# Optimization experiments

Measured on AMD Instinct MI355X. Metric: run time of the kernel, lower is better.

The kernel has to match this reference:

```python
import jax, jax.numpy as jnp
import numpy as np
from jax import lax

P = 16        # patch spatial size (C = 3 * P * P = 768)
CH = 3        # channels per patch
H = 8         # num attention heads
EPS_BN = 1e-3 # keras BatchNormalization default epsilon
EPS_LN = 1e-3 # keras LayerNormalization default epsilon


def _layernorm(x, g, b):
    mu = jnp.mean(x, axis=-1, keepdims=True)
    var = jnp.mean(jnp.square(x - mu), axis=-1, keepdims=True)
    return (x - mu) * lax.rsqrt(var + EPS_LN) * g + b


def setup_inputs() -> dict:
    key = jax.random.key(0)
    ks = jax.random.split(key, 8)
    B, N, C, DFF = 8, 1024, 768, 3072
    s = 0.02
    return {
        "encoded_patches": jax.random.normal(ks[0], (B, N, C), jnp.float32),
        "qconv_w": jax.random.normal(ks[1], (3, 3, CH, CH), jnp.float32) * 0.2,
        "reatten_w": jax.random.normal(ks[2], (H, H), jnp.float32) * 0.3,
        "reatten_b": jnp.zeros((H,), jnp.float32),
        "bn_gamma": jnp.ones((H,), jnp.float32),
        "bn_beta": jnp.zeros((H,), jnp.float32),
        "proj_w": jax.random.normal(ks[3], (C, C), jnp.float32) * s,
        "proj_b": jnp.zeros((C,), jnp.float32),
        "ffn_w1": jax.random.normal(ks[4], (C, DFF), jnp.float32) * s,
        "ffn_b1": jnp.zeros((DFF,), jnp.float32),
        "ffn_w2": jax.random.normal(ks[5], (DFF, C), jnp.float32) * s,
        "ffn_b2": jnp.zeros((C,), jnp.float32),
        "ln1_g": jnp.ones((C,), jnp.float32),
        "ln1_b": jnp.zeros((C,), jnp.float32),
        "ln2_g": jnp.ones((C,), jnp.float32),
        "ln2_b": jnp.zeros((C,), jnp.float32),
    }


def reference(encoded_patches, qconv_w, reatten_w, reatten_b, bn_gamma, bn_beta,
              proj_w, proj_b, ffn_w1, ffn_b1, ffn_w2, ffn_b2,
              ln1_g, ln1_b, ln2_g, ln2_b):
    B, N, C = encoded_patches.shape
    hd = C // H
    scale = jnp.float32(hd) ** -0.5

    # create_queries: unflatten [B,N,C] -> [B*N,P,P,CH], 3x3 'same' conv,
    # flatten back and split heads -> [B,H,N,hd]. Source uses qconv2d for
    # q, k AND v, so q == k == v; compute once.
    y = encoded_patches.reshape(B * N, P, P, CH)
    y = lax.conv_general_dilated(y, qconv_w, (1, 1), 'SAME',
                                 dimension_numbers=('NHWC', 'HWIO', 'NHWC'))
    q = y.reshape(B, N, H, hd).transpose(0, 2, 1, 3)  # [B,H,N,hd]
    k = q
    v = q

    # attention scores + softmax: [B,H,N,N]
    attn = jax.nn.softmax(jnp.einsum('bhnd,bhmd->bhnm', q, k) * scale, axis=-1)

    # re-attention: 1x1 conv mixing heads + BatchNorm (inference: mean=0, var=1)
    attn = jnp.einsum('bhnm,gh->bgnm', attn, reatten_w) + reatten_b[None, :, None, None]
    bn_s = bn_gamma * lax.rsqrt(jnp.float32(1.0) + EPS_BN)
    attn = attn * bn_s[None, :, None, None] + bn_beta[None, :, None, None]
    # reatten_scale = 1.0 (transform_scale=False)

    x = jnp.einsum('bhnm,bhmd->bhnd', attn, v)        # [B,H,N,hd]
    x = x.transpose(0, 2, 1, 3).reshape(B, N, C)
    x = x @ proj_w + proj_b

    x = x + encoded_patches          # residual
    x = _layernorm(x, ln1_g, ln1_b)  # LN1

    h = jax.nn.gelu(x @ ffn_w1 + ffn_b1, approximate=False)
    x = (h @ ffn_w2 + ffn_b2) + x    # FFN + residual
    x = _layernorm(x, ln2_g, ln2_b)  # LN2
    return x
```

## Files before the change

kernel.cpp:

```cpp
#include <hip/hip_runtime.h>
#include <hip/hip_bf16.h>
#include <math.h>

#define B_ 8
#define N_ 1024
#define C_ 768
#define H_ 8
#define HD_ 96
#define DFF_ 3072
#define SCALE_ 0.10206207261596575f

typedef __attribute__((ext_vector_type(8))) short bf16x8;
typedef __attribute__((ext_vector_type(4))) float f32x4;
typedef __attribute__((ext_vector_type(4))) short sh4;

__device__ __forceinline__ short f2bf(float f){
  __hip_bfloat16 h = __float2bfloat16(f);
  return __builtin_bit_cast(short, h);
}
__device__ __forceinline__ float bf2f(short s){
  unsigned u = ((unsigned)(unsigned short)s) << 16;
  return __builtin_bit_cast(float, u);
}
#define MFMA16(a,b,c) __builtin_amdgcn_mfma_f32_16x16x32_bf16((a),(b),(c),0,0,0)

__global__ void conv_q_kernel(const float* __restrict__ x, const float* __restrict__ w,
                              short* __restrict__ qb){
  int p = blockIdx.x;
  int t = threadIdx.x;
  __shared__ float xs[768];
  __shared__ float ws[81];
  const float* xp = x + (size_t)p * 768;
  xs[t] = xp[t]; xs[t+256] = xp[t+256]; xs[t+512] = xp[t+512];
  if (t < 81) ws[t] = w[t];
  __syncthreads();
  int i = t >> 4, j = t & 15;
  float a0=0.f, a1=0.f, a2=0.f;
  #pragma unroll
  for (int di=0; di<3; ++di){
    int ii = i + di - 1;
    if (ii < 0 || ii > 15) continue;
    #pragma unroll
    for (int dj=0; dj<3; ++dj){
      int jj = j + dj - 1;
      if (jj < 0 || jj > 15) continue;
      const float* cell = &xs[(ii*16+jj)*3];
      const float* wp = &ws[(di*3+dj)*9];
      #pragma unroll
      for (int ci=0; ci<3; ++ci){
        float xv = cell[ci];
        a0 += xv * wp[ci*3+0];
        a1 += xv * wp[ci*3+1];
        a2 += xv * wp[ci*3+2];
      }
    }
  }
  short* qp = qb + (size_t)p*768 + t*3;
  qp[0]=f2bf(a0); qp[1]=f2bf(a1); qp[2]=f2bf(a2);
}

__global__ void vt_kernel(const short* __restrict__ in, short* __restrict__ out){
  __shared__ short tile[32][33];
  int b = blockIdx.z;
  int c0 = blockIdx.x*32, n0 = blockIdx.y*32;
  int t = threadIdx.x;
  const short* ib = in + (size_t)b*N_*C_;
  short* ob = out + (size_t)b*C_*N_;
  #pragma unroll
  for (int i=0;i<4;i++){
    int idx = i*256+t; int r = idx>>5, cc = idx&31;
    tile[r][cc] = ib[(size_t)(n0+r)*C_ + c0+cc];
  }
  __syncthreads();
  #pragma unroll
  for (int i=0;i<4;i++){
    int idx = i*256+t; int r = idx>>5, cc = idx&31;
    ob[(size_t)(c0+r)*N_ + n0+cc] = tile[cc][r];
  }
}

__global__ void wtrans_kernel(const float* __restrict__ in, short* __restrict__ out,
                              int K, int Nn){
  __shared__ float tile[32][33];
  int n0 = blockIdx.x*32, k0 = blockIdx.y*32;
  int t = threadIdx.x;
  #pragma unroll
  for (int i=0;i<4;i++){
    int idx=i*256+t; int r=idx>>5, cc=idx&31;
    tile[r][cc] = in[(size_t)(k0+r)*Nn + n0+cc];
  }
  __syncthreads();
  #pragma unroll
  for (int i=0;i<4;i++){
    int idx=i*256+t; int r=idx>>5, cc=idx&31;
    out[(size_t)(n0+r)*K + k0+cc] = f2bf(tile[cc][r]);
  }
}

__global__ __launch_bounds__(512, 2)
void attn_kernel(const short* __restrict__ qb, const short* __restrict__ vt,
                 const float* __restrict__ rw, const float* __restrict__ rb,
                 const float* __restrict__ bng, const float* __restrict__ bnb,
                 short* __restrict__ out)
{
  __shared__ short P_lds[8][32][72];
  int b = blockIdx.x >> 5;
  int n0 = (blockIdx.x & 31) * 32;
  int tid = threadIdx.x;
  int w = tid >> 6;
  int l = tid & 63;
  int lg = l >> 4, lr = l & 15;
  const short* qbase = qb + (size_t)b*N_*C_;
  const short* vbase = vt + (size_t)b*C_*N_;

  bf16x8 qf[2][3];
  #pragma unroll
  for (int a=0;a<2;++a)
    #pragma unroll
    for (int kc=0;kc<3;++kc)
      qf[a][kc] = *(const bf16x8*)(qbase + (size_t)(n0+a*16+lr)*C_ + w*HD_ + kc*32 + lg*8);

  float bns = bng[w] * rsqrtf(1.0f + 1e-3f);
  float wmix[8];
  #pragma unroll
  for (int h=0;h<8;++h) wmix[h] = rw[w*8+h] * bns;
  float cw = rb[w]*bns + bnb[w];

  float mrun[2][4], lrun[2][4];
  #pragma unroll
  for (int a=0;a<2;++a)
    #pragma unroll
    for (int r=0;r<4;++r){ mrun[a][r] = -1e30f; lrun[a][r] = 0.f; }

  for (int mt=0; mt<16; ++mt){
    int m0 = mt*64;
    f32x4 sacc[2][4];
    #pragma unroll
    for (int a=0;a<2;++a)
      #pragma unroll
      for (int nt=0;nt<4;++nt) sacc[a][nt] = (f32x4){0.f,0.f,0.f,0.f};
    #pragma unroll
    for (int nt=0;nt<4;++nt){
      bf16x8 kf[3];
      #pragma unroll
      for (int kc=0;kc<3;++kc)
        kf[kc] = *(const bf16x8*)(qbase + (size_t)(m0+nt*16+lr)*C_ + w*HD_ + kc*32 + lg*8);
      #pragma unroll
      for (int kc=0;kc<3;++kc){
        sacc[0][nt] = MFMA16(qf[0][kc], kf[kc], sacc[0][nt]);
        sacc[1][nt] = MFMA16(qf[1][kc], kf[kc], sacc[1][nt]);
      }
    }
    #pragma unroll
    for (int a=0;a<2;++a){
      #pragma unroll
      for (int r=0;r<4;++r){
        float tm = fmaxf(fmaxf(sacc[a][0][r], sacc[a][1][r]),
                         fmaxf(sacc[a][2][r], sacc[a][3][r]));
        #pragma unroll
        for (int off=1; off<16; off<<=1) tm = fmaxf(tm, __shfl_xor(tm, off));
        tm *= SCALE_;
        float mn = fmaxf(mrun[a][r], tm);
        float s = 0.f;
        #pragma unroll
        for (int nt=0;nt<4;++nt) s += __expf(sacc[a][nt][r]*SCALE_ - mn);
        #pragma unroll
        for (int off=1; off<16; off<<=1) s += __shfl_xor(s, off);
        lrun[a][r] = lrun[a][r]*__expf(mrun[a][r]-mn) + s;
        mrun[a][r] = mn;
      }
    }
  }
  float invl[2][4];
  #pragma unroll
  for (int a=0;a<2;++a)
    #pragma unroll
    for (int r=0;r<4;++r) invl[a][r] = 1.0f / lrun[a][r];

  f32x4 oacc[2][6];
  #pragma unroll
  for (int a=0;a<2;++a)
    #pragma unroll
    for (int nt=0;nt<6;++nt) oacc[a][nt] = (f32x4){0.f,0.f,0.f,0.f};

  for (int mt=0; mt<16; ++mt){
    int m0 = mt*64;
    f32x4 sacc[2][4];
    #pragma unroll
    for (int a=0;a<2;++a)
      #pragma unroll
      for (int nt=0;nt<4;++nt) sacc[a][nt] = (f32x4){0.f,0.f,0.f,0.f};
    #pragma unroll
    for (int nt=0;nt<4;++nt){
      bf16x8 kf[3];
      #pragma unroll
      for (int kc=0;kc<3;++kc)
        kf[kc] = *(const bf16x8*)(qbase + (size_t)(m0+nt*16+lr)*C_ + w*HD_ + kc*32 + lg*8);
      #pragma unroll
      for (int kc=0;kc<3;++kc){
        sacc[0][nt] = MFMA16(qf[0][kc], kf[kc], sacc[0][nt]);
        sacc[1][nt] = MFMA16(qf[1][kc], kf[kc], sacc[1][nt]);
      }
    }
    __syncthreads();
    #pragma unroll
    for (int a=0;a<2;++a)
      #pragma unroll
      for (int nt=0;nt<4;++nt)
        #pragma unroll
        for (int r=0;r<4;++r){
          float p = __expf(sacc[a][nt][r]*SCALE_ - mrun[a][r]) * invl[a][r];
          P_lds[w][a*16 + lg*4 + r][nt*16 + lr] = f2bf(p);
        }
    __syncthreads();
    #pragma unroll
    for (int kc=0;kc<2;++kc){
      bf16x8 amix[2];
      #pragma unroll
      for (int a=0;a<2;++a){
        float pm[8];
        #pragma unroll
        for (int j=0;j<8;++j) pm[j] = cw;
        #pragma unroll
        for (int h=0;h<8;++h){
          bf16x8 ph = *(const bf16x8*)&P_lds[h][a*16+lr][kc*32+lg*8];
          #pragma unroll
          for (int j=0;j<8;++j) pm[j] += wmix[h]*bf2f(ph[j]);
        }
        #pragma unroll
        for (int j=0;j<8;++j) amix[a][j] = f2bf(pm[j]);
      }
      bf16x8 vf[6];
      #pragma unroll
      for (int nt=0;nt<6;++nt)
        vf[nt] = *(const bf16x8*)(vbase + (size_t)(w*HD_+nt*16+lr)*N_ + m0 + kc*32 + lg*8);
      #pragma unroll
      for (int nt=0;nt<6;++nt){
        oacc[0][nt] = MFMA16(amix[0], vf[nt], oacc[0][nt]);
        oacc[1][nt] = MFMA16(amix[1], vf[nt], oacc[1][nt]);
      }
    }
  }
  short* obase = out + (size_t)b*N_*C_;
  #pragma unroll
  for (int a=0;a<2;++a)
    #pragma unroll
    for (int nt=0;nt<6;++nt)
      #pragma unroll
      for (int r=0;r<4;++r)
        obase[(size_t)(n0 + a*16 + lg*4 + r)*C_ + w*HD_ + nt*16 + lr] = f2bf(oacc[a][nt][r]);
}

template<int EPI>
__global__ __launch_bounds__(256, 3)
void gemm_bt_kernel(const short* __restrict__ A, const short* __restrict__ Bt,
                    const float* __restrict__ bias, const float* __restrict__ res,
                    float* __restrict__ Of, short* __restrict__ Ob,
                    int M, int Nn, int K)
{
  __shared__ short As[128*72];
  __shared__ short Bs[128*72];
  int gm = blockIdx.y*128, gn = blockIdx.x*128;
  int tid = threadIdx.x;
  int w = tid>>6, l = tid&63, lg = l>>4, lr = l&15;
  int wr = w>>1, wc = w&1;
  f32x4 acc[4][4];
  #pragma unroll
  for (int mt=0;mt<4;++mt)
    #pragma unroll
    for (int nt=0;nt<4;++nt) acc[mt][nt] = (f32x4){0.f,0.f,0.f,0.f};

  bf16x8 ra[4], rbv[4];
  #pragma unroll
  for (int i=0;i<4;i++){
    int c = i*256+tid; int row = c>>3, cc = c&7;
    ra[i]  = *(const bf16x8*)(A  + (size_t)(gm+row)*K + cc*8);
    rbv[i] = *(const bf16x8*)(Bt + (size_t)(gn+row)*K + cc*8);
  }
  for (int kb=0; kb<K; kb+=64){
    __syncthreads();
    #pragma unroll
    for (int i=0;i<4;i++){
      int c = i*256+tid; int row=c>>3, cc=c&7;
      *(bf16x8*)&As[row*72 + cc*8] = ra[i];
      *(bf16x8*)&Bs[row*72 + cc*8] = rbv[i];
    }
    __syncthreads();
    if (kb + 64 < K){
      #pragma unroll
      for (int i=0;i<4;i++){
        int c=i*256+tid; int row=c>>3, cc=c&7;
        ra[i]  = *(const bf16x8*)(A  + (size_t)(gm+row)*K + kb+64 + cc*8);
        rbv[i] = *(const bf16x8*)(Bt + (size_t)(gn+row)*K + kb+64 + cc*8);
      }
    }
    #pragma unroll
    for (int kc=0;kc<2;++kc){
      bf16x8 af[4], bfr[4];
      #pragma unroll
      for (int mt=0;mt<4;++mt)
        af[mt] = *(const bf16x8*)&As[(wr*64+mt*16+lr)*72 + kc*32 + lg*8];
      #pragma unroll
      for (int nt=0;nt<4;++nt)
        bfr[nt] = *(const bf16x8*)&Bs[(wc*64+nt*16+lr)*72 + kc*32 + lg*8];
      #pragma unroll
      for (int mt=0;mt<4;++mt)
        #pragma unroll
        for (int nt=0;nt<4;++nt)
          acc[mt][nt] = MFMA16(af[mt], bfr[nt], acc[mt][nt]);
    }
  }
  #pragma unroll
  for (int mt=0;mt<4;++mt){
    #pragma unroll
    for (int nt=0;nt<4;++nt){
      #pragma unroll
      for (int r=0;r<4;++r){
        int row = gm + wr*64 + mt*16 + lg*4 + r;
        int col = gn + wc*64 + nt*16 + lr;
        float v = acc[mt][nt][r] + bias[col];
        if (EPI == 0){
          v += res[(size_t)row*Nn + col];
          Of[(size_t)row*Nn + col] = v;
        } else {
          v = 0.5f*v*(1.0f + erff(v*0.70710678118654752f));
          Ob[(size_t)row*Nn + col] = f2bf(v);
        }
      }
    }
  }
}

template<int WB>
__global__ void ln_kernel(const float* __restrict__ in, const float* __restrict__ gam,
                          const float* __restrict__ bet, float* __restrict__ of,
                          short* __restrict__ ob)
{
  int row = blockIdx.x*4 + (threadIdx.x>>6);
  int l = threadIdx.x & 63;
  const float* ip = in + (size_t)row*C_;
  float v[12];
  #pragma unroll
  for (int i=0;i<3;i++) *(float4*)&v[i*4] = *(const float4*)(ip + i*256 + l*4);
  float s = 0.f;
  #pragma unroll
  for (int i=0;i<12;i++) s += v[i];
  #pragma unroll
  for (int off=1; off<64; off<<=1) s += __shfl_xor(s, off);
  float mu = s * (1.0f/768.0f);
  float q = 0.f;
  #pragma unroll
  for (int i=0;i<12;i++){ float d = v[i]-mu; q += d*d; }
  #pragma unroll
  for (int off=1; off<64; off<<=1) q += __shfl_xor(q, off);
  float rstd = rsqrtf(q*(1.0f/768.0f) + 1e-3f);
  #pragma unroll
  for (int i=0;i<3;i++){
    float4 gv = *(const float4*)(gam + i*256 + l*4);
    float4 bv = *(const float4*)(bet + i*256 + l*4);
    float o0 = (v[i*4+0]-mu)*rstd*gv.x + bv.x;
    float o1 = (v[i*4+1]-mu)*rstd*gv.y + bv.y;
    float o2 = (v[i*4+2]-mu)*rstd*gv.z + bv.z;
    float o3 = (v[i*4+3]-mu)*rstd*gv.w + bv.w;
    float4 ov = {o0,o1,o2,o3};
    *(float4*)(of + (size_t)row*C_ + i*256 + l*4) = ov;
    if (WB){
      sh4 obv = { f2bf(o0), f2bf(o1), f2bf(o2), f2bf(o3) };
      *(sh4*)(ob + (size_t)row*C_ + i*256 + l*4) = obv;
    }
  }
}

extern "C" void kernel_launch(void* const* d_in, const int* in_sizes, int n_in,
                              void* d_out, int out_size, void* d_ws, size_t ws_size,
                              hipStream_t stream)
{
  const float* enc       = (const float*)d_in[0];
  const float* qconv_w   = (const float*)d_in[1];
  const float* reatten_w = (const float*)d_in[2];
  const float* reatten_b = (const float*)d_in[3];
  const float* bn_gamma  = (const float*)d_in[4];
  const float* bn_beta   = (const float*)d_in[5];
  const float* proj_w    = (const float*)d_in[6];
  const float* proj_b    = (const float*)d_in[7];
  const float* ffn_w1    = (const float*)d_in[8];
  const float* ffn_b1    = (const float*)d_in[9];
  const float* ffn_w2    = (const float*)d_in[10];
  const float* ffn_b2    = (const float*)d_in[11];
  const float* ln1_g     = (const float*)d_in[12];
  const float* ln1_b     = (const float*)d_in[13];
  const float* ln2_g     = (const float*)d_in[14];
  const float* ln2_b     = (const float*)d_in[15];
  float* outp = (float*)d_out;

  char* ws = (char*)d_ws;
  short* qbuf  = (short*)(ws);
  short* vtbuf = (short*)(ws + 12582912);
  short* atbuf = (short*)(ws + 25165824);
  float* ypre  = (float*)(ws + 37748736);
  float* x1    = (float*)(ws + 62914560);
  short* x1b   = (short*)(ws + 88080384);
  short* hbuf  = (short*)(ws + 100663296);
  short* wpt   = (short*)(ws + 150994944);
  short* w1t   = (short*)(ws + 152174592);
  short* w2t   = (short*)(ws + 156893184);

  conv_q_kernel<<<B_*N_, 256, 0, stream>>>(enc, qconv_w, qbuf);
  vt_kernel<<<dim3(C_/32, N_/32, B_), 256, 0, stream>>>(qbuf, vtbuf);
  wtrans_kernel<<<dim3(C_/32,  C_/32), 256, 0, stream>>>(proj_w, wpt, C_,  C_);
  wtrans_kernel<<<dim3(DFF_/32, C_/32), 256, 0, stream>>>(ffn_w1, w1t, C_,  DFF_);
  wtrans_kernel<<<dim3(C_/32, DFF_/32), 256, 0, stream>>>(ffn_w2, w2t, DFF_, C_);
  attn_kernel<<<B_*(N_/32), 512, 0, stream>>>(qbuf, vtbuf, reatten_w, reatten_b,
                                              bn_gamma, bn_beta, atbuf);
  gemm_bt_kernel<0><<<dim3(C_/128, (B_*N_)/128), 256, 0, stream>>>(
      atbuf, wpt, proj_b, enc, ypre, nullptr, B_*N_, C_, C_);
  ln_kernel<1><<<(B_*N_)/4, 256, 0, stream>>>(ypre, ln1_g, ln1_b, x1, x1b);
  gemm_bt_kernel<1><<<dim3(DFF_/128, (B_*N_)/128), 256, 0, stream>>>(
      x1b, w1t, ffn_b1, nullptr, nullptr, hbuf, B_*N_, DFF_, C_);
  gemm_bt_kernel<0><<<dim3(C_/128, (B_*N_)/128), 256, 0, stream>>>(
      hbuf, w2t, ffn_b2, x1, ypre, nullptr, B_*N_, C_, DFF_);
  ln_kernel<0><<<(B_*N_)/4, 256, 0, stream>>>(ypre, ln2_g, ln2_b, outp, nullptr);
}
```

Baseline: 373.8 us.

## Split attention keys across two wave groups and use direct-to-LDS GEMM loads

The attention kernel now launches 1024 threads per block. Two groups of 8 waves each process half of the key range. Their softmax max and sum statistics are merged through LDS, and their partial outputs are combined at the end. The score MFMA operands are swapped so each lane owns a whole query row, which removes most shuffle reductions, and the P tile uses an XOR-swizzled LDS layout. The GEMM replaces register-staged prefetch with global_load_lds into a swizzled unpadded tile, but it now waits on each load before computing, so the software overlap is lost; occupancy hints are also raised.

Result: slower. 530.8 us (+42.0%).

```diff
diff --git a/kernel.cpp b/kernel.cpp
--- a/kernel.cpp
+++ b/kernel.cpp
@@ -23,6 +23,11 @@
   return __builtin_bit_cast(float, u);
 }
 #define MFMA16(a,b,c) __builtin_amdgcn_mfma_f32_16x16x32_bf16((a),(b),(c),0,0,0)
+
+__device__ __forceinline__ void gload16(const void* g, void* l){
+  __builtin_amdgcn_global_load_lds((const __attribute__((address_space(1))) unsigned int*)g,
+                                   (__attribute__((address_space(3))) unsigned int*)l, 16, 0, 0);
+}
 
 __global__ void conv_q_kernel(const float* __restrict__ x, const float* __restrict__ w,
                               short* __restrict__ qb){
@@ -97,19 +102,19 @@
   }
 }
 
-__global__ __launch_bounds__(512, 2)
+__global__ __launch_bounds__(1024, 4)
 void attn_kernel(const short* __restrict__ qb, const short* __restrict__ vt,
                  const float* __restrict__ rw, const float* __restrict__ rb,
                  const float* __restrict__ bng, const float* __restrict__ bnb,
                  short* __restrict__ out)
 {
-  __shared__ short P_lds[8][32][72];
+  __shared__ short Pl[32768];
   int b = blockIdx.x >> 5;
   int n0 = (blockIdx.x & 31) * 32;
   int tid = threadIdx.x;
-  int w = tid >> 6;
-  int l = tid & 63;
-  int lg = l >> 4, lr = l & 15;
+  int w16 = tid >> 6;
+  int h = w16 & 7, seg = w16 >> 3;
+  int l = tid & 63, lg = l >> 4, lr = l & 15;
   const short* qbase = qb + (size_t)b*N_*C_;
   const short* vbase = vt + (size_t)b*C_*N_;
 
@@ -118,114 +123,134 @@
   for (int a=0;a<2;++a)
     #pragma unroll
     for (int kc=0;kc<3;++kc)
-      qf[a][kc] = *(const bf16x8*)(qbase + (size_t)(n0+a*16+lr)*C_ + w*HD_ + kc*32 + lg*8);
-
-  float bns = bng[w] * rsqrtf(1.0f + 1e-3f);
+      qf[a][kc] = *(const bf16x8*)(qbase + (size_t)(n0+a*16+lr)*C_ + h*HD_ + kc*32 + lg*8);
+
+  float bns = bng[h] * rsqrtf(1.001f);
   float wmix[8];
   #pragma unroll
-  for (int h=0;h<8;++h) wmix[h] = rw[w*8+h] * bns;
-  float cw = rb[w]*bns + bnb[w];
-
-  float mrun[2][4], lrun[2][4];
+  for (int hh=0;hh<8;++hh) wmix[hh] = rw[h*8+hh] * bns;
+  float cw = rb[h]*bns + bnb[h];
+
+  float mrun[2] = {-1e30f, -1e30f}, lrun[2] = {0.f, 0.f};
+
+  for (int mt=0; mt<8; ++mt){
+    int m0 = (seg*8 + mt)*64;
+    f32x4 sacc[2][4];
+    #pragma unroll
+    for (int a=0;a<2;++a)
+      #pragma unroll
+      for (int s=0;s<4;++s) sacc[a][s] = (f32x4){0.f,0.f,0.f,0.f};
+    #pragma unroll
+    for (int s=0;s<4;++s){
+      bf16x8 kf[3];
+      #pragma unroll
+      for (int kc=0;kc<3;++kc)
+        kf[kc] = *(const bf16x8*)(qbase + (size_t)(m0+s*16+lr)*C_ + h*HD_ + kc*32 + lg*8);
+      #pragma unroll
+      for (int kc=0;kc<3;++kc){
+        sacc[0][s] = MFMA16(kf[kc], qf[0][kc], sacc[0][s]);
+        sacc[1][s] = MFMA16(kf[kc], qf[1][kc], sacc[1][s]);
+      }
+    }
+    #pragma unroll
+    for (int a=0;a<2;++a){
+      float tm = -1e30f;
+      #pragma unroll
+      for (int s=0;s<4;++s)
+        #pragma unroll
+        for (int r=0;r<4;++r) tm = fmaxf(tm, sacc[a][s][r]);
+      tm = fmaxf(tm, __shfl_xor(tm, 16));
+      tm = fmaxf(tm, __shfl_xor(tm, 32));
+      tm *= SCALE_;
+      float mn = fmaxf(mrun[a], tm);
+      float ss = 0.f;
+      #pragma unroll
+      for (int s=0;s<4;++s)
+        #pragma unroll
+        for (int r=0;r<4;++r) ss += __expf(sacc[a][s][r]*SCALE_ - mn);
+      ss += __shfl_xor(ss, 16);
+      ss += __shfl_xor(ss, 32);
+      lrun[a] = lrun[a]*__expf(mrun[a]-mn) + ss;
+      mrun[a] = mn;
+    }
+  }
+
+  float* sm = (float*)Pl;
+  float* sl = sm + 1024;
+  if (l < 16){
+    #pragma unroll
+    for (int a=0;a<2;++a){
+      sm[((h*2+seg)*2+a)*16 + l] = mrun[a];
+      sl[((h*2+seg)*2+a)*16 + l] = lrun[a];
+    }
+  }
+  __syncthreads();
+  float mf[2], invl[2];
+  #pragma unroll
+  for (int a=0;a<2;++a){
+    float mo = sm[((h*2+(seg^1))*2+a)*16 + lr];
+    float lo = sl[((h*2+(seg^1))*2+a)*16 + lr];
+    float mm = fmaxf(mrun[a], mo);
+    float lf = lrun[a]*__expf(mrun[a]-mm) + lo*__expf(mo-mm);
+    mf[a] = mm;
+    invl[a] = 1.0f / lf;
+  }
+
+  f32x4 oacc[2][6];
   #pragma unroll
   for (int a=0;a<2;++a)
     #pragma unroll
-    for (int r=0;r<4;++r){ mrun[a][r] = -1e30f; lrun[a][r] = 0.f; }
-
-  for (int mt=0; mt<16; ++mt){
-    int m0 = mt*64;
+    for (int nt=0;nt<6;++nt) oacc[a][nt] = (f32x4){0.f,0.f,0.f,0.f};
+
+  for (int mt=0; mt<8; ++mt){
+    int m0 = (seg*8 + mt)*64;
     f32x4 sacc[2][4];
     #pragma unroll
     for (int a=0;a<2;++a)
       #pragma unroll
-      for (int nt=0;nt<4;++nt) sacc[a][nt] = (f32x4){0.f,0.f,0.f,0.f};
-    #pragma unroll
-    for (int nt=0;nt<4;++nt){
+      for (int s=0;s<4;++s) sacc[a][s] = (f32x4){0.f,0.f,0.f,0.f};
+    #pragma unroll
+    for (int s=0;s<4;++s){
       bf16x8 kf[3];
       #pragma unroll
       for (int kc=0;kc<3;++kc)
-        kf[kc] = *(const bf16x8*)(qbase + (size_t)(m0+nt*16+lr)*C_ + w*HD_ + kc*32 + lg*8);
+        kf[kc] = *(const bf16x8*)(qbase + (size_t)(m0+s*16+lr)*C_ + h*HD_ + kc*32 + lg*8);
       #pragma unroll
       for (int kc=0;kc<3;++kc){
-        sacc[0][nt] = MFMA16(qf[0][kc], kf[kc], sacc[0][nt]);
-        sacc[1][nt] = MFMA16(qf[1][kc], kf[kc], sacc[1][nt]);
-      }
-    }
+        sacc[0][s] = MFMA16(kf[kc], qf[0][kc], sacc[0][s]);
+        sacc[1][s] = MFMA16(kf[kc], qf[1][kc], sacc[1][s]);
+      }
+    }
+    __syncthreads();
     #pragma unroll
     for (int a=0;a<2;++a){
-      #pragma unroll
-      for (int r=0;r<4;++r){
-        float tm = fmaxf(fmaxf(sacc[a][0][r], sacc[a][1][r]),
-                         fmaxf(sacc[a][2][r], sacc[a][3][r]));
-        #pragma unroll
-        for (int off=1; off<16; off<<=1) tm = fmaxf(tm, __shfl_xor(tm, off));
-        tm *= SCALE_;
-        float mn = fmaxf(mrun[a][r], tm);
-        float s = 0.f;
-        #pragma unroll
-        for (int nt=0;nt<4;++nt) s += __expf(sacc[a][nt][r]*SCALE_ - mn);
-        #pragma unroll
-        for (int off=1; off<16; off<<=1) s += __shfl_xor(s, off);
-        lrun[a][r] = lrun[a][r]*__expf(mrun[a][r]-mn) + s;
-        mrun[a][r] = mn;
-      }
-    }
-  }
-  float invl[2][4];
-  #pragma unroll
-  for (int a=0;a<2;++a)
-    #pragma unroll
-    for (int r=0;r<4;++r) invl[a][r] = 1.0f / lrun[a][r];
-
-  f32x4 oacc[2][6];
-  #pragma unroll
-  for (int a=0;a<2;++a)
-    #pragma unroll
-    for (int nt=0;nt<6;++nt) oacc[a][nt] = (f32x4){0.f,0.f,0.f,0.f};
-
-  for (int mt=0; mt<16; ++mt){
-    int m0 = mt*64;
-    f32x4 sacc[2][4];
-    #pragma unroll
-    for (int a=0;a<2;++a)
-      #pragma unroll
-      for (int nt=0;nt<4;++nt) sacc[a][nt] = (f32x4){0.f,0.f,0.f,0.f};
-    #pragma unroll
-    for (int nt=0;nt<4;++nt){
-      bf16x8 kf[3];
-      #pragma unroll
-      for (int kc=0;kc<3;++kc)
-        kf[kc] = *(const bf16x8*)(qbase + (size_t)(m0+nt*16+lr)*C_ + w*HD_ + kc*32 + lg*8);
-      #pragma unroll
-      for (int kc=0;kc<3;++kc){
-        sacc[0][nt] = MFMA16(qf[0][kc], kf[kc], sacc[0][nt]);
-        sacc[1][nt] = MFMA16(qf[1][kc], kf[kc], sacc[1][nt]);
-      }
-    }
-    __syncthreads();
-    #pragma unroll
-    for (int a=0;a<2;++a)
-      #pragma unroll
-      for (int nt=0;nt<4;++nt)
-        #pragma unroll
-        for (int r=0;r<4;++r){
-          float p = __expf(sacc[a][nt][r]*SCALE_ - mrun[a][r]) * invl[a][r];
-          P_lds[w][a*16 + lg*4 + r][nt*16 + lr] = f2bf(p);
-        }
+      int row = a*16 + lr;
+      #pragma unroll
+      for (int s=0;s<4;++s){
+        sh4 pv;
+        #pragma unroll
+        for (int r=0;r<4;++r)
+          pv[r] = f2bf(__expf(sacc[a][s][r]*SCALE_ - mf[a]) * invl[a]);
+        int wp = (s*2 + (lg>>1)) ^ (lr&7);
+        *(sh4*)&Pl[seg*16384 + (h*32+row)*64 + wp*8 + (lg&1)*4] = pv;
+      }
+    }
     __syncthreads();
     #pragma unroll
     for (int kc=0;kc<2;++kc){
       bf16x8 amix[2];
       #pragma unroll
       for (int a=0;a<2;++a){
+        int row = a*16 + lr;
         float pm[8];
         #pragma unroll
         for (int j=0;j<8;++j) pm[j] = cw;
         #pragma unroll
-        for (int h=0;h<8;++h){
-          bf16x8 ph = *(const bf16x8*)&P_lds[h][a*16+lr][kc*32+lg*8];
+        for (int hh=0;hh<8;++hh){
+          int wp = (kc*4 + lg) ^ (lr&7);
+          bf16x8 ph = *(const bf16x8*)&Pl[seg*16384 + (hh*32+row)*64 + wp*8];
           #pragma unroll
-          for (int j=0;j<8;++j) pm[j] += wmix[h]*bf2f(ph[j]);
+          for (int j=0;j<8;++j) pm[j] += wmix[hh]*bf2f(ph[j]);
         }
         #pragma unroll
         for (int j=0;j<8;++j) amix[a][j] = f2bf(pm[j]);
@@ -233,7 +258,7 @@
       bf16x8 vf[6];
       #pragma unroll
       for (int nt=0;nt<6;++nt)
-        vf[nt] = *(const bf16x8*)(vbase + (size_t)(w*HD_+nt*16+lr)*N_ + m0 + kc*32 + lg*8);
+        vf[nt] = *(const bf16x8*)(vbase + (size_t)(h*HD_+nt*16+lr)*N_ + m0 + kc*32 + lg*8);
       #pragma unroll
       for (int nt=0;nt<6;++nt){
         oacc[0][nt] = MFMA16(amix[0], vf[nt], oacc[0][nt]);
@@ -241,68 +266,80 @@
       }
     }
   }
-  short* obase = out + (size_t)b*N_*C_;
-  #pragma unroll
-  for (int a=0;a<2;++a)
-    #pragma unroll
-    for (int nt=0;nt<6;++nt)
-      #pragma unroll
-      for (int r=0;r<4;++r)
-        obase[(size_t)(n0 + a*16 + lg*4 + r)*C_ + w*HD_ + nt*16 + lr] = f2bf(oacc[a][nt][r]);
+
+  __syncthreads();
+  short* mrg = Pl;
+  if (seg == 1){
+    #pragma unroll
+    for (int a=0;a<2;++a)
+      #pragma unroll
+      for (int nt=0;nt<6;++nt)
+        #pragma unroll
+        for (int r=0;r<4;++r)
+          mrg[(h*32 + a*16 + lg*4 + r)*100 + nt*16 + lr] = f2bf(oacc[a][nt][r]);
+  }
+  __syncthreads();
+  if (seg == 0){
+    short* obase = out + (size_t)b*N_*C_;
+    #pragma unroll
+    for (int a=0;a<2;++a)
+      #pragma unroll
+      for (int nt=0;nt<6;++nt)
+        #pragma unroll
+        for (int r=0;r<4;++r){
+          float v = oacc[a][nt][r] + bf2f(mrg[(h*32 + a*16 + lg*4 + r)*100 + nt*16 + lr]);
+          obase[(size_t)(n0 + a*16 + lg*4 + r)*C_ + h*HD_ + nt*16 + lr] = f2bf(v);
+        }
+  }
 }
 
 template<int EPI>
-__global__ __launch_bounds__(256, 3)
+__global__ __launch_bounds__(256, 4)
 void gemm_bt_kernel(const short* __restrict__ A, const short* __restrict__ Bt,
                     const float* __restrict__ bias, const float* __restrict__ res,
                     float* __restrict__ Of, short* __restrict__ Ob,
                     int M, int Nn, int K)
 {
-  __shared__ short As[128*72];
-  __shared__ short Bs[128*72];
+  __shared__ short As[8192];
+  __shared__ short Bs[8192];
   int gm = blockIdx.y*128, gn = blockIdx.x*128;
   int tid = threadIdx.x;
   int w = tid>>6, l = tid&63, lg = l>>4, lr = l&15;
   int wr = w>>1, wc = w&1;
+  int srow = l>>3;
+  int wlog = (l&7) ^ srow;
   f32x4 acc[4][4];
   #pragma unroll
   for (int mt=0;mt<4;++mt)
     #pragma unroll
     for (int nt=0;nt<4;++nt) acc[mt][nt] = (f32x4){0.f,0.f,0.f,0.f};
 
-  bf16x8 ra[4], rbv[4];
-  #pragma unroll
-  for (int i=0;i<4;i++){
-    int c = i*256+tid; int row = c>>3, cc = c&7;
-    ra[i]  = *(const bf16x8*)(A  + (size_t)(gm+row)*K + cc*8);
-    rbv[i] = *(const bf16x8*)(Bt + (size_t)(gn+row)*K + cc*8);
-  }
+  const short* Asrc = A + (size_t)gm*K;
+  const short* Bsrc = Bt + (size_t)gn*K;
+
   for (int kb=0; kb<K; kb+=64){
     __syncthreads();
     #pragma unroll
-    for (int i=0;i<4;i++){
-      int c = i*256+tid; int row=c>>3, cc=c&7;
-      *(bf16x8*)&As[row*72 + cc*8] = ra[i];
-      *(bf16x8*)&Bs[row*72 + cc*8] = rbv[i];
-    }
+    for (int j=0;j<4;++j){
+      int c = w*4+j;
+      gload16(Asrc + (size_t)(c*8+srow)*K + kb + wlog*8, &As[c*512]);
+      gload16(Bsrc + (size_t)(c*8+srow)*K + kb + wlog*8, &Bs[c*512]);
+    }
+    asm volatile("s_waitcnt vmcnt(0)" ::: "memory");
     __syncthreads();
-    if (kb + 64 < K){
-      #pragma unroll
-      for (int i=0;i<4;i++){
-        int c=i*256+tid; int row=c>>3, cc=c&7;
-        ra[i]  = *(const bf16x8*)(A  + (size_t)(gm+row)*K + kb+64 + cc*8);
-        rbv[i] = *(const bf16x8*)(Bt + (size_t)(gn+row)*K + kb+64 + cc*8);
-      }
-    }
     #pragma unroll
     for (int kc=0;kc<2;++kc){
       bf16x8 af[4], bfr[4];
       #pragma unroll
-      for (int mt=0;mt<4;++mt)
-        af[mt] = *(const bf16x8*)&As[(wr*64+mt*16+lr)*72 + kc*32 + lg*8];
-      #pragma unroll
-      for (int nt=0;nt<4;++nt)
-        bfr[nt] = *(const bf16x8*)&Bs[(wc*64+nt*16+lr)*72 + kc*32 + lg*8];
+      for (int mt=0;mt<4;++mt){
+        int row = wr*64+mt*16+lr;
+        af[mt] = *(const bf16x8*)&As[row*64 + (((kc*4+lg)^(lr&7))*8)];
+      }
+      #pragma unroll
+      for (int nt=0;nt<4;++nt){
+        int row = wc*64+nt*16+lr;
+        bfr[nt] = *(const bf16x8*)&Bs[row*64 + (((kc*4+lg)^(lr&7))*8)];
+      }
       #pragma unroll
       for (int mt=0;mt<4;++mt)
         #pragma unroll
@@ -410,8 +447,8 @@
   wtrans_kernel<<<dim3(C_/32,  C_/32), 256, 0, stream>>>(proj_w, wpt, C_,  C_);
   wtrans_kernel<<<dim3(DFF_/32, C_/32), 256, 0, stream>>>(ffn_w1, w1t, C_,  DFF_);
   wtrans_kernel<<<dim3(C_/32, DFF_/32), 256, 0, stream>>>(ffn_w2, w2t, DFF_, C_);
-  attn_kernel<<<B_*(N_/32), 512, 0, stream>>>(qbuf, vtbuf, reatten_w, reatten_b,
-                                              bn_gamma, bn_beta, atbuf);
+  attn_kernel<<<B_*(N_/32), 1024, 0, stream>>>(qbuf, vtbuf, reatten_w, reatten_b,
+                                               bn_gamma, bn_beta, atbuf);
   gemm_bt_kernel<0><<<dim3(C_/128, (B_*N_)/128), 256, 0, stream>>>(
       atbuf, wpt, proj_b, enc, ypre, nullptr, B_*N_, C_, C_);
   ln_kernel<1><<<(B_*N_)/4, 256, 0, stream>>>(ypre, ln1_g, ln1_b, x1, x1b);
```
